# Optimization experiments

Measured on AMD Instinct MI355X. Metric: run time of the kernel, lower is better.

Reference implementation:

```python
import jax, jax.numpy as jnp
import numpy as np

HEADS = 8
BN_EPS = 1e-5


def setup_inputs() -> dict:
    B, S, D = 8, 1024, 512
    key = jax.random.key(0)
    ks = jax.random.split(key, 4)
    x = jax.random.normal(ks[0], (B, S, D), dtype=jnp.float32)
    scale = 0.02
    Wq = jax.random.normal(ks[1], (D, D), dtype=jnp.float32) * scale
    Wk = jax.random.normal(ks[2], (D, D), dtype=jnp.float32) * scale
    Wv = jax.random.normal(ks[3], (D, D), dtype=jnp.float32) * scale
    zeros = jnp.zeros((D,), dtype=jnp.float32)
    return {
        "x": x,
        "Wq": Wq, "bq": zeros,
        "Wk": Wk, "bk": zeros,
        "Wv": Wv, "bv": zeros,
        "gamma": jnp.ones((D,), dtype=jnp.float32),
        "beta": zeros,
    }


def reference(x, Wq, bq, Wk, bk, Wv, bv, gamma, beta):
    # x: [B, S, D]
    B, S, D = x.shape
    H = HEADS
    dh = D // H

    Q = jax.nn.relu(jnp.einsum('bsd,de->bse', x, Wq) + bq).reshape(B, S, H, dh)
    K = jax.nn.relu(jnp.einsum('bsd,de->bse', x, Wk) + bk).reshape(B, S, H, dh)
    V = jax.nn.relu(jnp.einsum('bsd,de->bse', x, Wv) + bv).reshape(B, S, H, dh)

    # torch split(dim=2)+cat(dim=0) == per-head batched attention; scores [B,H,q,k]
    scores = jnp.einsum('bqhd,bkhd->bhqk', Q, K) / jnp.sqrt(jnp.float32(dh))
    # NOTE: original uses F.softmax(output, dim=1) on [H*B, S, S]; dim=1 is the
    # QUERY axis (non-standard), i.e. axis 2 of [b,h,q,k].
    attn = jax.nn.softmax(scores, axis=2)
    # dropout omitted (deterministic / eval mode)
    out = jnp.einsum('bhqk,bkhd->bqhd', attn, V).reshape(B, S, D)

    y = out + x  # residual

    # BatchNorm1d (training mode): per-channel stats over (B, S), biased var
    mean = jnp.mean(y, axis=(0, 1))
    var = jnp.mean(jnp.square(y - mean), axis=(0, 1))
    y = (y - mean) * jax.lax.rsqrt(var + BN_EPS) * gamma + beta
    return y
```

## Files before the change

kernel.cpp:

```cpp
#include <hip/hip_runtime.h>
#include <hip/hip_bf16.h>
#include <math.h>

typedef __bf16 bf16;
typedef __bf16 bf16x8 __attribute__((ext_vector_type(8)));
typedef float floatx4 __attribute__((ext_vector_type(4)));

#define NB 8
#define NS 1024
#define ND 512
#define NH 8
#define NDH 64
#define NBH 64
#define MROWS 8192
#define N3 1536
#define KSCL 0.18033688f

#define GLD16(src, dst)                                                            \
    __builtin_amdgcn_global_load_lds(                                              \
        (const __attribute__((address_space(1))) void*)(src),                      \
        (__attribute__((address_space(3))) void*)(dst), 16, 0, 0)

static __device__ __forceinline__ floatx4 mfma16(bf16x8 a, bf16x8 b, floatx4 c) {
    return __builtin_amdgcn_mfma_f32_16x16x32_bf16(a, b, c, 0, 0, 0);
}

static __device__ __forceinline__ float fexp2(float x) {
#if __has_builtin(__builtin_amdgcn_exp2f)
    return __builtin_amdgcn_exp2f(x);
#else
    return __expf(x * 0.69314718f);
#endif
}

static __device__ __forceinline__ unsigned pack2(float lo, float hi) {
    union { bf16 h[2]; unsigned u; } u;
    u.h[0] = (bf16)lo; u.h[1] = (bf16)hi;
    return u.u;
}

static __device__ __forceinline__ void plane32(unsigned &a, unsigned &b) {
    asm("v_permlane32_swap_b32 %0, %1" : "+v"(a), "+v"(b));
}
static __device__ __forceinline__ void plane16(unsigned &a, unsigned &b) {
    asm("v_permlane16_swap_b32 %0, %1" : "+v"(a), "+v"(b));
}

__global__ void prep(const float* __restrict__ x, bf16* __restrict__ xb,
                     float* __restrict__ bnSum, const float* __restrict__ Wq,
                     const float* __restrict__ Wk, const float* __restrict__ Wv,
                     bf16* __restrict__ Wb) {
    __shared__ float tl[32][33];
    int bid = blockIdx.x;
    int t = threadIdx.x;
    if (bid < 2048) {
        if (bid == 0) {
            ((float4*)bnSum)[t] = make_float4(0.f, 0.f, 0.f, 0.f);
        }
        int i = (bid * 256 + t) * 8;
        float4 a = *(const float4*)&x[i];
        float4 b = *(const float4*)&x[i + 4];
        bf16 o[8] = {(bf16)a.x, (bf16)a.y, (bf16)a.z, (bf16)a.w,
                     (bf16)b.x, (bf16)b.y, (bf16)b.z, (bf16)b.w};
        *(bf16x8*)&xb[i] = *(bf16x8*)o;
    } else {
        int wbid = bid - 2048;
        int mat = wbid >> 8;
        int bx = wbid & 15;
        int by = (wbid >> 4) & 15;
        const float* W = mat == 0 ? Wq : (mat == 1 ? Wk : Wv);
        int d0 = bx * 32, e0 = by * 32;
        int tx = t & 31, ty = t >> 5;
#pragma unroll
        for (int i = 0; i < 4; i++) tl[ty * 4 + i][tx] = W[(d0 + ty * 4 + i) * ND + e0 + tx];
        __syncthreads();
#pragma unroll
        for (int i = 0; i < 4; i++)
            Wb[(mat * ND + e0 + ty * 4 + i) * ND + d0 + tx] = (bf16)tl[tx][ty * 4 + i];
    }
}

__launch_bounds__(256)
__global__ void gemm1(const bf16* __restrict__ xb, const bf16* __restrict__ Wb,
                      const float* __restrict__ bq, const float* __restrict__ bk,
                      const float* __restrict__ bv, bf16* __restrict__ QKV) {
    __shared__ __align__(16) bf16 As[128 * 64];
    __shared__ __align__(16) bf16 Bs[128 * 64];
    int t = threadIdx.x, lane = t & 63, w = t >> 6;
    int wr = w >> 1, wc = w & 1;
    int lr = lane & 15, lg = lane >> 4;
    int row0 = blockIdx.x * 128, col0 = blockIdx.y * 128;
    int srow = t >> 3, sj = t & 7;
    floatx4 acc[4][4] = {};
    for (int k0 = 0; k0 < ND; k0 += 64) {
        __syncthreads();
#pragma unroll
        for (int it = 0; it < 4; it++) {
            int row = it * 32 + srow;
            int j = sj ^ (row & 7);
            GLD16(&xb[(size_t)(row0 + row) * ND + k0 + j * 8], &As[(it * 256 + w * 64) * 8]);
            GLD16(&Wb[(size_t)(col0 + row) * ND + k0 + j * 8], &Bs[(it * 256 + w * 64) * 8]);
        }
        __syncthreads();
        bf16x8 af[2][4], bfr[2][4];
#pragma unroll
        for (int ks = 0; ks < 2; ks++) {
#pragma unroll
            for (int mt = 0; mt < 4; mt++)
                af[ks][mt] = *(const bf16x8*)&As[(wr * 64 + mt * 16 + lr) * 64 +
                                                 ((ks * 4 + lg) ^ (lr & 7)) * 8];
#pragma unroll
            for (int nt = 0; nt < 4; nt++)
                bfr[ks][nt] = *(const bf16x8*)&Bs[(wc * 64 + nt * 16 + lr) * 64 +
                                                  ((ks * 4 + lg) ^ (lr & 7)) * 8];
        }
#pragma unroll
        for (int ks = 0; ks < 2; ks++)
#pragma unroll
            for (int mt = 0; mt < 4; mt++)
#pragma unroll
                for (int nt = 0; nt < 4; nt++)
                    acc[mt][nt] = mfma16(af[ks][mt], bfr[ks][nt], acc[mt][nt]);
    }
#pragma unroll
    for (int mt = 0; mt < 4; mt++)
#pragma unroll
        for (int nt = 0; nt < 4; nt++) {
            int col = col0 + wc * 64 + nt * 16 + lr;
            float bias = col < 512 ? bq[col] : (col < 1024 ? bk[col - 512] : bv[col - 1024]);
            float scl = (col >= 512 && col < 1024) ? KSCL : 1.0f;
#pragma unroll
            for (int r = 0; r < 4; r++) {
                int row = row0 + wr * 64 + mt * 16 + lg * 4 + r;
                float v = acc[mt][nt][r] + bias;
                v = v > 0.f ? v : 0.f;
                v *= scl;
                QKV[(size_t)row * N3 + col] = (bf16)v;
            }
        }
}

__launch_bounds__(256)
__global__ void attn_colsum_vt(const bf16* __restrict__ QKV, bf16* __restrict__ VB) {
    __shared__ __align__(16) bf16 Qs[128 * 64];
    __shared__ float rcS[128];
    int bh = blockIdx.x, b = bh >> 3, h = bh & 7;
    int k0 = blockIdx.y * 128;
    int t = threadIdx.x, lane = t & 63, w = t >> 6;
    int lr = lane & 15, lg = lane >> 4;
    int srow = t >> 3, sj = t & 7;
    bf16x8 kf[2][2];
#pragma unroll
    for (int tt = 0; tt < 2; tt++)
#pragma unroll
        for (int s = 0; s < 2; s++)
            kf[tt][s] = *(const bf16x8*)&QKV[(size_t)(b * NS + k0 + w * 32 + tt * 16 + lr) * N3 +
                                             512 + h * NDH + s * 32 + lg * 8];
    floatx4 csum[2] = {};
    const floatx4 zf = {};
    for (int qc = 0; qc < 8; qc++) {
        __syncthreads();
#pragma unroll
        for (int it = 0; it < 4; it++) {
            int row = it * 32 + srow;
            int j = sj ^ (row & 7);
            GLD16(&QKV[(size_t)(b * NS + qc * 128 + row) * N3 + h * NDH + j * 8],
                  &Qs[(it * 256 + w * 64) * 8]);
        }
        __syncthreads();
        __builtin_amdgcn_s_setprio(1);
#pragma unroll
        for (int qt = 0; qt < 8; qt++) {
            bf16x8 qb0 = *(const bf16x8*)&Qs[(qt * 16 + lr) * 64 + (lg ^ (lr & 7)) * 8];
            bf16x8 qb1 = *(const bf16x8*)&Qs[(qt * 16 + lr) * 64 + ((4 + lg) ^ (lr & 7)) * 8];
#pragma unroll
            for (int tt = 0; tt < 2; tt++) {
                floatx4 a = mfma16(kf[tt][0], qb0, zf);
                a = mfma16(kf[tt][1], qb1, a);
#pragma unroll
                for (int r = 0; r < 4; r++) csum[tt][r] += fexp2(a[r]);
            }
        }
        __builtin_amdgcn_s_setprio(0);
    }
#pragma unroll
    for (int tt = 0; tt < 2; tt++)
#pragma unroll
        for (int r = 0; r < 4; r++) {
            float v = csum[tt][r];
            v += __shfl_xor(v, 1);
            v += __shfl_xor(v, 2);
            v += __shfl_xor(v, 4);
            v += __shfl_xor(v, 8);
            csum[tt][r] = v;
        }
    if (lr == 0) {
#pragma unroll
        for (int tt = 0; tt < 2; tt++)
#pragma unroll
            for (int r = 0; r < 4; r++)
                rcS[w * 32 + tt * 16 + lg * 4 + r] = 1.f / csum[tt][r];
    }
    __syncthreads();
#pragma unroll
    for (int it = 0; it < 4; it++) {
        int row = it * 32 + srow;
        int j = sj ^ (row & 7);
        GLD16(&QKV[(size_t)(b * NS + k0 + row) * N3 + 1024 + h * NDH + j * 8],
              &Qs[(it * 256 + w * 64) * 8]);
    }
    __syncthreads();
#pragma unroll
    for (int nt = 0; nt < 4; nt++) {
        int d = nt * 16 + lr;
        bf16 tmp[8];
#pragma unroll
        for (int j = 0; j < 8; j++) {
            int row = w * 32 + lg * 8 + j;
            float v = (float)Qs[row * 64 + (((d >> 3) ^ (row & 7)) * 8) + (d & 7)];
            tmp[j] = (bf16)(v * rcS[row]);
        }
        size_t blob = (size_t)((bh * 32 + (k0 >> 5) + w) * 4 + nt);
        *(bf16x8*)&VB[blob * 512 + lane * 8] = *(bf16x8*)tmp;
    }
}

__launch_bounds__(256)
__global__ void attn_fused(bf16* __restrict__ QKV, const bf16* __restrict__ VB,
                           const float* __restrict__ x,
                           float* __restrict__ bnSum, float* __restrict__ bnSumSq) {
    __shared__ __align__(16) bf16 Ks[128 * 64];
    int bh = blockIdx.x, b = bh >> 3, h = bh & 7;
    int q0 = blockIdx.y * 128;
    int t = threadIdx.x, lane = t & 63, w = t >> 6;
    int lr = lane & 15, lg = lane >> 4;
    bf16x8 qf[2][2];
#pragma unroll
    for (int n = 0; n < 2; n++)
#pragma unroll
        for (int s = 0; s < 2; s++)
            qf[n][s] = *(const bf16x8*)&QKV[(size_t)(b * NS + q0 + w * 32 + n * 16 + lr) * N3 +
                                            h * NDH + s * 32 + lg * 8];
    const bf16* vbase = &VB[(size_t)(bh * 32) * 4 * 512 + lane * 8];
    int sKrow = t >> 3, sKj = t & 7;
    floatx4 oacc[2][4] = {};
    const floatx4 zf = {};
    for (int kb = 0; kb < 8; kb++) {
        int k0 = kb * 128;
        __syncthreads();
#pragma unroll
        for (int it = 0; it < 4; it++) {
            int rowK = it * 32 + sKrow;
            int jK = sKj ^ (rowK & 7);
            GLD16(&QKV[(size_t)(b * NS + k0 + rowK) * N3 + 512 + h * NDH + jK * 8],
                  &Ks[(it * 256 + w * 64) * 8]);
        }
        __syncthreads();
        __builtin_amdgcn_s_setprio(1);
#pragma unroll
        for (int kt = 0; kt < 4; kt++) {
            bf16x8 kfr[2][2];
#pragma unroll
            for (int tt = 0; tt < 2; tt++)
#pragma unroll
                for (int s = 0; s < 2; s++)
                    kfr[tt][s] = *(const bf16x8*)&Ks[(kt * 32 + tt * 16 + lr) * 64 +
                                                     ((s * 4 + lg) ^ (lr & 7)) * 8];
            bf16x8 vf[4];
#pragma unroll
            for (int nt = 0; nt < 4; nt++)
                vf[nt] = *(const bf16x8*)&vbase[(size_t)((kb * 4 + kt) * 4 + nt) * 512];
#pragma unroll
            for (int n = 0; n < 2; n++) {
                floatx4 s0 = mfma16(kfr[0][0], qf[n][0], zf);
                s0 = mfma16(kfr[0][1], qf[n][1], s0);
                floatx4 s1 = mfma16(kfr[1][0], qf[n][0], zf);
                s1 = mfma16(kfr[1][1], qf[n][1], s1);
                float e0[4], e1[4];
#pragma unroll
                for (int r = 0; r < 4; r++) {
                    e0[r] = fexp2(s0[r]);
                    e1[r] = fexp2(s1[r]);
                }
                unsigned A0 = pack2(e0[0], e0[1]);
                unsigned A1 = pack2(e0[2], e0[3]);
                unsigned B0 = pack2(e1[0], e1[1]);
                unsigned B1 = pack2(e1[2], e1[3]);
                plane32(A0, B0); plane16(A0, B0);
                plane32(A1, B1); plane16(A1, B1);
                union { unsigned u[4]; bf16x8 v; } af;
                af.u[0] = A0; af.u[1] = A1; af.u[2] = B0; af.u[3] = B1;
#pragma unroll
                for (int nt = 0; nt < 4; nt++)
                    oacc[n][nt] = mfma16(af.v, vf[nt], oacc[n][nt]);
            }
        }
        __builtin_amdgcn_s_setprio(0);
    }
    float bs[4] = {}, bq2[4] = {};
#pragma unroll
    for (int n = 0; n < 2; n++)
#pragma unroll
        for (int nt = 0; nt < 4; nt++) {
            int d = nt * 16 + lr;
#pragma unroll
            for (int r = 0; r < 4; r++) {
                int q = q0 + w * 32 + n * 16 + lg * 4 + r;
                size_t row = (size_t)(b * NS + q);
                float yv = oacc[n][nt][r] + x[row * ND + h * NDH + d];
                QKV[row * N3 + 1024 + h * NDH + d] = (bf16)yv;
                bs[nt] += yv;
                bq2[nt] += yv * yv;
            }
        }
#pragma unroll
    for (int nt = 0; nt < 4; nt++) {
        float v = bs[nt], q2 = bq2[nt];
        v += __shfl_xor(v, 16); v += __shfl_xor(v, 32);
        q2 += __shfl_xor(q2, 16); q2 += __shfl_xor(q2, 32);
        if (lg == 0) {
            atomicAdd(&bnSum[h * NDH + nt * 16 + lr], v);
            atomicAdd(&bnSumSq[h * NDH + nt * 16 + lr], q2);
        }
    }
}

__global__ void bn_apply(const bf16* __restrict__ QKV, float* __restrict__ y,
                         const float* __restrict__ bnSum, const float* __restrict__ bnSumSq,
                         const float* __restrict__ gamma, const float* __restrict__ beta) {
    int i = (blockIdx.x * 256 + threadIdx.x) * 8;
    int row = i >> 9, col = i & 511;
    bf16x8 yv = *(const bf16x8*)&QKV[(size_t)row * N3 + 1024 + col];
    float4 s0 = *(const float4*)&bnSum[col];
    float4 s1 = *(const float4*)&bnSum[col + 4];
    float4 q0 = *(const float4*)&bnSumSq[col];
    float4 q1 = *(const float4*)&bnSumSq[col + 4];
    float4 g0 = *(const float4*)&gamma[col];
    float4 g1 = *(const float4*)&gamma[col + 4];
    float4 b0 = *(const float4*)&beta[col];
    float4 b1 = *(const float4*)&beta[col + 4];
    float sm[8] = {s0.x, s0.y, s0.z, s0.w, s1.x, s1.y, s1.z, s1.w};
    float sq[8] = {q0.x, q0.y, q0.z, q0.w, q1.x, q1.y, q1.z, q1.w};
    float gm[8] = {g0.x, g0.y, g0.z, g0.w, g1.x, g1.y, g1.z, g1.w};
    float bt[8] = {b0.x, b0.y, b0.z, b0.w, b1.x, b1.y, b1.z, b1.w};
    float out[8];
#pragma unroll
    for (int j = 0; j < 8; j++) {
        float mean = sm[j] * (1.f / 8192.f);
        float var = sq[j] * (1.f / 8192.f) - mean * mean;
        float rstd = rsqrtf(var + 1e-5f);
        out[j] = ((float)yv[j] - mean) * rstd * gm[j] + bt[j];
    }
    *(float4*)&y[i] = make_float4(out[0], out[1], out[2], out[3]);
    *(float4*)&y[i + 4] = make_float4(out[4], out[5], out[6], out[7]);
}

extern "C" void kernel_launch(void* const* d_in, const int* in_sizes, int n_in,
                              void* d_out, int out_size, void* d_ws, size_t ws_size,
                              hipStream_t stream) {
    const float* x  = (const float*)d_in[0];
    const float* Wq = (const float*)d_in[1];
    const float* bq = (const float*)d_in[2];
    const float* Wk = (const float*)d_in[3];
    const float* bk = (const float*)d_in[4];
    const float* Wv = (const float*)d_in[5];
    const float* bv = (const float*)d_in[6];
    const float* gamma = (const float*)d_in[7];
    const float* beta  = (const float*)d_in[8];
    float* y = (float*)d_out;

    char* ws = (char*)d_ws;
    const size_t WB_OFF  = 0;
    const size_t QKV_OFF = 2u << 20;
    const size_t VT_OFF  = QKV_OFF + (size_t)MROWS * N3 * 2;
    const size_t BN_OFF  = VT_OFF + (size_t)NBH * NDH * NS * 2;
    const size_t XB_OFF  = BN_OFF + (4u << 12);
    bf16*  Wb     = (bf16*)(ws + WB_OFF);
    bf16*  QKV    = (bf16*)(ws + QKV_OFF);
    bf16*  VB     = (bf16*)(ws + VT_OFF);
    float* bnSum  = (float*)(ws + BN_OFF);
    float* bnSumSq = bnSum + 512;
    bf16*  xb     = (bf16*)(ws + XB_OFF);

    prep<<<2816, 256, 0, stream>>>(x, xb, bnSum, Wq, Wk, Wv, Wb);
    gemm1<<<dim3(64, 12), 256, 0, stream>>>(xb, Wb, bq, bk, bv, QKV);
    attn_colsum_vt<<<dim3(64, 8), 256, 0, stream>>>(QKV, VB);
    attn_fused<<<dim3(64, 8), 256, 0, stream>>>(QKV, VB, x, bnSum, bnSumSq);
    bn_apply<<<2048, 256, 0, stream>>>(QKV, y, bnSum, bnSumSq, gamma, beta);
}
```

Before: 81.86 us.

## Prepack K into fragment-major blobs and load directly from global in attention

The colsum kernel now writes each wave's K MFMA fragments into a fragment-major buffer, KB, which reuses the xb workspace. The fused attention kernel then reads K fragments straight from global memory with coalesced 16-byte loads per lane. This removes the LDS staging of K along with the two barriers per key block. In exchange, every wave re-reads K from global or L2 instead of sharing it through LDS, and there is no explicit prefetch overlap.

New measurement: 84.64 us. 3.4% more time.

```diff
diff --git a/kernel.cpp b/kernel.cpp
--- a/kernel.cpp
+++ b/kernel.cpp
@@ -141,11 +141,13 @@
 }
 
 __launch_bounds__(256)
-__global__ void attn_colsum_vt(const bf16* __restrict__ QKV, bf16* __restrict__ VB) {
+__global__ void attn_colsum_vt(const bf16* __restrict__ QKV, bf16* __restrict__ VB,
+                               bf16* __restrict__ KB) {
     __shared__ __align__(16) bf16 Qs[128 * 64];
     __shared__ float rcS[128];
     int bh = blockIdx.x, b = bh >> 3, h = bh & 7;
-    int k0 = blockIdx.y * 128;
+    int kbidx = blockIdx.y;
+    int k0 = kbidx * 128;
     int t = threadIdx.x, lane = t & 63, w = t >> 6;
     int lr = lane & 15, lg = lane >> 4;
     int srow = t >> 3, sj = t & 7;
@@ -156,6 +158,12 @@
         for (int s = 0; s < 2; s++)
             kf[tt][s] = *(const bf16x8*)&QKV[(size_t)(b * NS + k0 + w * 32 + tt * 16 + lr) * N3 +
                                              512 + h * NDH + s * 32 + lg * 8];
+#pragma unroll
+    for (int tt = 0; tt < 2; tt++)
+#pragma unroll
+        for (int s = 0; s < 2; s++)
+            *(bf16x8*)&KB[(size_t)((((bh * 8 + kbidx) * 4 + w) * 4) + tt * 2 + s) * 512 +
+                          lane * 8] = kf[tt][s];
     floatx4 csum[2] = {};
     const floatx4 zf = {};
     for (int qc = 0; qc < 8; qc++) {
@@ -220,16 +228,15 @@
             float v = (float)Qs[row * 64 + (((d >> 3) ^ (row & 7)) * 8) + (d & 7)];
             tmp[j] = (bf16)(v * rcS[row]);
         }
-        size_t blob = (size_t)((bh * 32 + (k0 >> 5) + w) * 4 + nt);
+        size_t blob = (size_t)((bh * 32 + kbidx * 4 + w) * 4 + nt);
         *(bf16x8*)&VB[blob * 512 + lane * 8] = *(bf16x8*)tmp;
     }
 }
 
 __launch_bounds__(256)
 __global__ void attn_fused(bf16* __restrict__ QKV, const bf16* __restrict__ VB,
-                           const float* __restrict__ x,
+                           const bf16* __restrict__ KB, const float* __restrict__ x,
                            float* __restrict__ bnSum, float* __restrict__ bnSumSq) {
-    __shared__ __align__(16) bf16 Ks[128 * 64];
     int bh = blockIdx.x, b = bh >> 3, h = bh & 7;
     int q0 = blockIdx.y * 128;
     int t = threadIdx.x, lane = t & 63, w = t >> 6;
@@ -242,20 +249,10 @@
             qf[n][s] = *(const bf16x8*)&QKV[(size_t)(b * NS + q0 + w * 32 + n * 16 + lr) * N3 +
                                             h * NDH + s * 32 + lg * 8];
     const bf16* vbase = &VB[(size_t)(bh * 32) * 4 * 512 + lane * 8];
-    int sKrow = t >> 3, sKj = t & 7;
+    const bf16* kbase = &KB[(size_t)(bh * 8) * 16 * 512 + lane * 8];
     floatx4 oacc[2][4] = {};
     const floatx4 zf = {};
     for (int kb = 0; kb < 8; kb++) {
-        int k0 = kb * 128;
-        __syncthreads();
-#pragma unroll
-        for (int it = 0; it < 4; it++) {
-            int rowK = it * 32 + sKrow;
-            int jK = sKj ^ (rowK & 7);
-            GLD16(&QKV[(size_t)(b * NS + k0 + rowK) * N3 + 512 + h * NDH + jK * 8],
-                  &Ks[(it * 256 + w * 64) * 8]);
-        }
-        __syncthreads();
         __builtin_amdgcn_s_setprio(1);
 #pragma unroll
         for (int kt = 0; kt < 4; kt++) {
@@ -264,8 +261,8 @@
             for (int tt = 0; tt < 2; tt++)
 #pragma unroll
                 for (int s = 0; s < 2; s++)
-                    kfr[tt][s] = *(const bf16x8*)&Ks[(kt * 32 + tt * 16 + lr) * 64 +
-                                                     ((s * 4 + lg) ^ (lr & 7)) * 8];
+                    kfr[tt][s] = *(const bf16x8*)&kbase[(size_t)(((kb * 4 + kt) * 4) +
+                                                                 tt * 2 + s) * 512];
             bf16x8 vf[4];
 #pragma unroll
             for (int nt = 0; nt < 4; nt++)
@@ -381,10 +378,11 @@
     float* bnSum  = (float*)(ws + BN_OFF);
     float* bnSumSq = bnSum + 512;
     bf16*  xb     = (bf16*)(ws + XB_OFF);
+    bf16*  KB     = xb;
 
     prep<<<2816, 256, 0, stream>>>(x, xb, bnSum, Wq, Wk, Wv, Wb);
     gemm1<<<dim3(64, 12), 256, 0, stream>>>(xb, Wb, bq, bk, bv, QKV);
-    attn_colsum_vt<<<dim3(64, 8), 256, 0, stream>>>(QKV, VB);
-    attn_fused<<<dim3(64, 8), 256, 0, stream>>>(QKV, VB, x, bnSum, bnSumSq);
+    attn_colsum_vt<<<dim3(64, 8), 256, 0, stream>>>(QKV, VB, KB);
+    attn_fused<<<dim3(64, 8), 256, 0, stream>>>(QKV, VB, KB, x, bnSum, bnSumSq);
     bn_apply<<<2048, 256, 0, stream>>>(QKV, y, bnSum, bnSumSq, gamma, beta);
 }
```
